# Performance work log

Measured on AMD Instinct MI355X. Metric: run time of the kernel, lower is better.

Reference implementation:

```python
import jax, jax.numpy as jnp
import numpy as np

# WikiText-103 adaptive softmax config
CUTOFFS = (0, 20000, 40000, 200000, 267735)  # cluster boundaries


def setup_inputs() -> dict:
    key = jax.random.key(0)
    ks = jax.random.split(key, 12)
    N, D = 1024, 1024
    rn = lambda k, shape, std: jax.random.normal(k, shape, jnp.float32) * std
    return {
        "hidden": jax.random.normal(ks[0], (N, D), jnp.float32),
        "target": jax.random.randint(ks[1], (N,), 0, CUTOFFS[-1], jnp.int32),
        "head_w": rn(ks[2], (20000, 1024), 0.02),
        "head_b": jnp.zeros((20000,), jnp.float32),
        "cluster_w": rn(ks[3], (3, 1024), 0.02),
        "cluster_b": jnp.zeros((3,), jnp.float32),
        "proj0": rn(ks[4], (1024, 1024), 0.01),
        "proj1": rn(ks[5], (1024, 256), 0.01),
        "proj2": rn(ks[6], (1024, 64), 0.01),
        "proj3": rn(ks[7], (1024, 16), 0.01),
        "w1": rn(ks[8], (20000, 256), 0.02),
        "b1": jnp.zeros((20000,), jnp.float32),
        "w2": rn(ks[9], (160000, 64), 0.02),
        "b2": jnp.zeros((160000,), jnp.float32),
        "w3": rn(ks[10], (67735, 16), 0.02),
        "b3": jnp.zeros((67735,), jnp.float32),
    }


def _logit(h, w, b, proj):
    # F.linear(F.linear(h, proj.t()), w, b) == (h @ proj) @ w.T + b
    return (h @ proj) @ w.T + b


def reference(hidden, target, head_w, head_b, cluster_w, cluster_b,
              proj0, proj1, proj2, proj3, w1, b1, w2, b2, w3, b3):
    # head: shortlist vocab (20000) + 3 cluster logits -> [N, 20003]
    hw = jnp.concatenate([head_w, cluster_w], axis=0)
    hb = jnp.concatenate([head_b, cluster_b], axis=0)
    head_lp = jax.nn.log_softmax(_logit(hidden, hw, hb, proj0), axis=-1)

    # cluster 0 (shortlist): logprob directly from head
    t0 = jnp.clip(target, 0, CUTOFFS[1] - 1)
    lp = jnp.take_along_axis(head_lp, t0[:, None].astype(jnp.int32), axis=1)[:, 0]

    tails = [(w1, b1, proj1), (w2, b2, proj2), (w3, b3, proj3)]
    for i, (w, b, p) in enumerate(tails, start=1):
        l, r = CUTOFFS[i], CUTOFFS[i + 1]
        mask = (target >= l) & (target < r)
        ti = jnp.clip(target - l, 0, r - l - 1)
        tail_lp = jax.nn.log_softmax(_logit(hidden, w, b, p), axis=-1)  # [N, r-l]
        # note: torch code indexes head_logprob[:, -i] (reversed cluster order quirk)
        lpi = head_lp[:, -i] + jnp.take_along_axis(tail_lp, ti[:, None], axis=1)[:, 0]
        lp = jnp.where(mask, lpi, lp)

    return -lp  # nll per token, keep_order semantics
```

## Files before the change

kernel.cpp:

```cpp
#include <hip/hip_runtime.h>
#include <math.h>

typedef __bf16 bf16;
typedef __bf16 bf16x4 __attribute__((ext_vector_type(4)));
typedef __bf16 bf16x8 __attribute__((ext_vector_type(8)));
typedef float  f32x4  __attribute__((ext_vector_type(4)));

__device__ __forceinline__ f32x4 mfma16x16x32(bf16x8 a, bf16x8 b, f32x4 c) {
  return __builtin_amdgcn_mfma_f32_16x16x32_bf16(a, b, c, 0, 0, 0);
}

__device__ __forceinline__ void async16(const bf16* gp, bf16* lp) {
  __builtin_amdgcn_global_load_lds(
      (const __attribute__((address_space(1))) void*)gp,
      (__attribute__((address_space(3))) void*)lp, 16, 0, 0);
}

__global__ void __launch_bounds__(256) convert_bf16_kernel(const float* __restrict__ in,
                                                           bf16* __restrict__ out, int n4) {
  int i = blockIdx.x * 256 + threadIdx.x;
  if (i < n4) {
    float4 f = ((const float4*)in)[i];
    bf16x4 b = {(bf16)f.x, (bf16)f.y, (bf16)f.z, (bf16)f.w};
    ((bf16x4*)out)[i] = b;
  }
}

__global__ void __launch_bounds__(256) convert_pad_kernel(const float* __restrict__ in,
                                                          bf16* __restrict__ out,
                                                          int n4, int n4tot) {
  int i = blockIdx.x * 256 + threadIdx.x;
  if (i >= n4tot) return;
  bf16x4 b = {(bf16)0.f, (bf16)0.f, (bf16)0.f, (bf16)0.f};
  if (i < n4) {
    float4 f = ((const float4*)in)[i];
    b = (bf16x4){(bf16)f.x, (bf16)f.y, (bf16)f.z, (bf16)f.w};
  }
  ((bf16x4*)out)[i] = b;
}

__global__ void __launch_bounds__(256) convert_w3_kernel(const float* __restrict__ w3,
                                                         bf16* __restrict__ W3b,
                                                         int n4, int n4tot) {
  int i = blockIdx.x * 256 + threadIdx.x;
  if (i >= n4tot) return;
  int row = i >> 2, kq = i & 3;
  bf16x4 z = {(bf16)0.f, (bf16)0.f, (bf16)0.f, (bf16)0.f};
  bf16x4 b = z;
  if (i < n4) {
    float4 f = *(const float4*)&w3[(size_t)i * 4];
    b = (bf16x4){(bf16)f.x, (bf16)f.y, (bf16)f.z, (bf16)f.w};
  }
  *(bf16x4*)&W3b[(size_t)row * 32 + kq * 4] = b;
  *(bf16x4*)&W3b[(size_t)row * 32 + 16 + kq * 4] = z;
}

__global__ void __launch_bounds__(256) transpose_convert_kernel(const float* __restrict__ P,
                                                                bf16* __restrict__ Pt, int dX) {
  __shared__ float t[32][33];
  int tx = threadIdx.x & 31, ty = threadIdx.x >> 5;
  int k0 = blockIdx.x * 32, c0 = blockIdx.y * 32;
#pragma unroll
  for (int s = 0; s < 4; ++s) {
    int k = k0 + ty + s * 8, col = c0 + tx;
    t[ty + s * 8][tx] = (col < dX) ? P[(size_t)k * dX + col] : 0.f;
  }
  __syncthreads();
#pragma unroll
  for (int s = 0; s < 4; ++s) {
    int colo = c0 + ty + s * 8;
    Pt[(size_t)colo * 1024 + k0 + tx] = (bf16)t[tx][ty + s * 8];
  }
}

__global__ void __launch_bounds__(1024) compact_kernel(const int* __restrict__ target,
                                                       int* __restrict__ rowmap,
                                                       int* __restrict__ slotmap,
                                                       int* __restrict__ counts) {
  __shared__ int cnt[3];
  int tid = threadIdx.x;
  if (tid < 3) cnt[tid] = 0;
  for (int i = tid; i < 3 * 1152; i += 1024) rowmap[i] = 0;
  __syncthreads();
  int t = target[tid];
  int c = (t >= 200000) ? 2 : (t >= 40000) ? 1 : (t >= 20000) ? 0 : -1;
  int slot = -1;
  if (c >= 0) {
    slot = atomicAdd(&cnt[c], 1);
    rowmap[c * 1152 + slot] = tid;
  }
  slotmap[tid] = slot;
  __syncthreads();
  if (tid < 3) counts[tid] = cnt[tid];
}

template <int KDIM, bool LSE>
__global__ void __launch_bounds__(256) gemm_kernel(
    const bf16* __restrict__ A, int strideA,
    const int* __restrict__ rmap, const int* __restrict__ cntp,
    const bf16* __restrict__ B,
    const float* __restrict__ bias, const float* __restrict__ bias2,
    int splice, int V, float* __restrict__ part, int nchunk,
    bf16* __restrict__ Out, int strideOut, int dX) {
  constexpr int BK = 64;
  constexpr int KG = BK / 8;
  constexpr int NIT = KDIM / BK;
  __shared__ bf16 Alds[2][128 * BK];
  __shared__ bf16 Blds[2][128 * BK];
  __shared__ float wpart[2][128];

  const int tid = threadIdx.x;
  const int w = tid >> 6, lane = tid & 63;
  const int q = lane >> 4, c = lane & 15;
  const int wr = w >> 1, wc = w & 1;

  int f = blockIdx.x;
  int xr = f & 7, rb = (f >> 3) & 7, cq = f >> 6;
  int chunk = cq * 8 + xr;
  if (chunk >= nchunk) return;
  const int row0 = rb * 128, col0 = chunk * 128;
  if (cntp && row0 >= *cntp) return;

  int arow[KG / 2];
#pragma unroll
  for (int i = 0; i < KG / 2; ++i) {
    int g = i * 256 + tid;
    int r = row0 + g / KG;
    arow[i] = rmap ? rmap[r] : r;
  }

  auto stage = [&](int kt, int pb) {
    const int k0 = kt * BK;
#pragma unroll
    for (int i = 0; i < KG / 2; ++i) {
      int g = i * 256 + tid;
      int col = g / KG, j = g % KG;
      int kg = j ^ (col & 7);
      async16(A + (size_t)arow[i] * strideA + k0 + kg * 8,
              &Alds[pb][(size_t)(g & ~63) * 8]);
      async16(B + (size_t)(col0 + col) * KDIM + k0 + kg * 8,
              &Blds[pb][(size_t)(g & ~63) * 8]);
    }
  };

  f32x4 acc[4][4] = {};

  stage(0, 0);
  __syncthreads();

  for (int kt = 0; kt < NIT; ++kt) {
    const int cb = kt & 1;
    if (kt + 1 < NIT) stage(kt + 1, cb ^ 1);
#pragma unroll
    for (int ks = 0; ks < BK / 32; ++ks) {
      bf16x8 af[4], bfr[4];
#pragma unroll
      for (int rt = 0; rt < 4; ++rt) {
        int rl = wr * 64 + rt * 16 + c;
        int kq = ks * 4 + q;
        int kg = kq ^ (rl & 7);
        af[rt] = *(const bf16x8*)&Alds[cb][((size_t)rl * KG + kg) * 8];
      }
#pragma unroll
      for (int ct = 0; ct < 4; ++ct) {
        int cl = wc * 64 + ct * 16 + c;
        int kq = ks * 4 + q;
        int kg = kq ^ (cl & 7);
        bfr[ct] = *(const bf16x8*)&Blds[cb][((size_t)cl * KG + kg) * 8];
      }
#pragma unroll
      for (int rt = 0; rt < 4; ++rt)
#pragma unroll
        for (int ct = 0; ct < 4; ++ct)
          acc[rt][ct] = mfma16x16x32(af[rt], bfr[ct], acc[rt][ct]);
    }
    __syncthreads();
  }

  if (!LSE) {
#pragma unroll
    for (int rt = 0; rt < 4; ++rt)
#pragma unroll
      for (int ct = 0; ct < 4; ++ct)
#pragma unroll
        for (int r = 0; r < 4; ++r) {
          int col = col0 + wc * 64 + ct * 16 + c;
          if (col < dX) {
            int row = row0 + wr * 64 + rt * 16 + q * 4 + r;
            Out[(size_t)row * strideOut + col] = (bf16)acc[rt][ct][r];
          }
        }
    return;
  }

  float bv[4];
#pragma unroll
  for (int ct = 0; ct < 4; ++ct) {
    int colg = col0 + wc * 64 + ct * 16 + c;
    bv[ct] = (colg < V) ? ((colg < splice) ? bias[colg] : bias2[colg - splice]) : -INFINITY;
  }
#pragma unroll
  for (int rt = 0; rt < 4; ++rt) {
#pragma unroll
    for (int r = 0; r < 4; ++r) {
      float s = 0.f;
#pragma unroll
      for (int ct = 0; ct < 4; ++ct) s += __expf(acc[rt][ct][r] + bv[ct]);
#pragma unroll
      for (int off = 1; off <= 8; off <<= 1) s += __shfl_xor(s, off);
      if (c == 0) wpart[wc][wr * 64 + rt * 16 + q * 4 + r] = s;
    }
  }
  __syncthreads();
  if (tid < 128)
    part[(size_t)chunk * 1024 + row0 + tid] = __logf(wpart[0][tid] + wpart[1][tid]);
}

template <int KDIM, int G>
__global__ void __launch_bounds__(256) gemm_lse_wide_kernel(
    const bf16* __restrict__ A, int strideA,
    const int* __restrict__ rmap, const int* __restrict__ cntp,
    const bf16* __restrict__ B, const float* __restrict__ bias,
    int V, float* __restrict__ part, int nchunk) {
  constexpr int BK = KDIM;
  constexpr int KG = BK / 8;
  constexpr int NL = KG / 2;
  __shared__ bf16 Alds[128 * BK];
  __shared__ bf16 Blds[3][128 * BK];
  __shared__ float biasl[G * 128];
  __shared__ float spart[2][128];

  const int tid = threadIdx.x;
  const int w = tid >> 6, lane = tid & 63;
  const int q = lane >> 4, c = lane & 15;
  const int wr = w >> 1, wc = w & 1;

  const int row0 = blockIdx.y * 128;
  if (row0 >= *cntp) return;
  const int chunk0 = blockIdx.x * G;
  const int nc = (nchunk - chunk0 < G) ? (nchunk - chunk0) : G;

  for (int i = tid; i < G * 128; i += 256) {
    int colg = chunk0 * 128 + i;
    biasl[i] = (colg < V) ? bias[colg] : -INFINITY;
  }
#pragma unroll
  for (int i = 0; i < NL; ++i) {
    int g = i * 256 + tid;
    int row = g / KG, j = g % KG;
    int kg = (KG == 8) ? (j ^ (row & 7)) : (j ^ ((row >> 1) & 3));
    int ar = rmap[row0 + row];
    async16(A + (size_t)ar * strideA + kg * 8, &Alds[(size_t)(g & ~63) * 8]);
  }
#pragma unroll
  for (int b = 0; b < 2; ++b) {
    int ck = (b < nc) ? b : nc - 1;
#pragma unroll
    for (int i = 0; i < NL; ++i) {
      int g = i * 256 + tid;
      int col = g / KG, j = g % KG;
      int kg = (KG == 8) ? (j ^ (col & 7)) : (j ^ ((col >> 1) & 3));
      async16(B + (size_t)((chunk0 + ck) * 128 + col) * KDIM + kg * 8,
              &Blds[b][(size_t)(g & ~63) * 8]);
    }
  }
  __syncthreads();

  bf16x8 af[BK / 32][4];
#pragma unroll
  for (int ks = 0; ks < BK / 32; ++ks)
#pragma unroll
    for (int rt = 0; rt < 4; ++rt) {
      int rl = wr * 64 + rt * 16 + c;
      int kq = ks * 4 + q;
      int kg = (KG == 8) ? (kq ^ (rl & 7)) : (kq ^ ((rl >> 1) & 3));
      af[ks][rt] = *(const bf16x8*)&Alds[((size_t)rl * KG + kg) * 8];
    }

  float sums[4][4] = {};
  int ib = 0;

  for (int ci = 0; ci < nc; ++ci) {
    {
      int pre = (ci + 2 < nc) ? ci + 2 : nc - 1;
      bf16* bw = Blds[(ib == 0) ? 2 : ib - 1];
#pragma unroll
      for (int i = 0; i < NL; ++i) {
        int g = i * 256 + tid;
        int col = g / KG, j = g % KG;
        int kg = (KG == 8) ? (j ^ (col & 7)) : (j ^ ((col >> 1) & 3));
        async16(B + (size_t)((chunk0 + pre) * 128 + col) * KDIM + kg * 8,
                &bw[(size_t)(g & ~63) * 8]);
      }
    }

    const bf16* Bl = Blds[ib];
    f32x4 acc[4][4] = {};
#pragma unroll
    for (int ks = 0; ks < BK / 32; ++ks) {
      bf16x8 bfr[4];
#pragma unroll
      for (int ct = 0; ct < 4; ++ct) {
        int cl = wc * 64 + ct * 16 + c;
        int kq = ks * 4 + q;
        int kg = (KG == 8) ? (kq ^ (cl & 7)) : (kq ^ ((cl >> 1) & 3));
        bfr[ct] = *(const bf16x8*)&Bl[((size_t)cl * KG + kg) * 8];
      }
#pragma unroll
      for (int rt = 0; rt < 4; ++rt)
#pragma unroll
        for (int ct = 0; ct < 4; ++ct)
          acc[rt][ct] = mfma16x16x32(af[ks][rt], bfr[ct], acc[rt][ct]);
    }

    float bv[4];
#pragma unroll
    for (int ct = 0; ct < 4; ++ct) bv[ct] = biasl[ci * 128 + wc * 64 + ct * 16 + c];
#pragma unroll
    for (int rt = 0; rt < 4; ++rt)
#pragma unroll
      for (int r = 0; r < 4; ++r) {
#pragma unroll
        for (int ct = 0; ct < 4; ++ct)
          sums[rt][r] += __expf(acc[rt][ct][r] + bv[ct]);
      }

    if constexpr (NL == 4) asm volatile("s_waitcnt vmcnt(4)" ::: "memory");
    else                   asm volatile("s_waitcnt vmcnt(2)" ::: "memory");
    __builtin_amdgcn_sched_barrier(0);
    __builtin_amdgcn_s_barrier();
    ib = (ib == 2) ? 0 : ib + 1;
  }

#pragma unroll
  for (int rt = 0; rt < 4; ++rt)
#pragma unroll
    for (int r = 0; r < 4; ++r) {
      float s = sums[rt][r];
#pragma unroll
      for (int off = 1; off <= 8; off <<= 1) s += __shfl_xor(s, off);
      if (c == 0) spart[wc][wr * 64 + rt * 16 + q * 4 + r] = s;
    }
  __syncthreads();
  if (tid < 128)
    part[(size_t)blockIdx.x * 1024 + row0 + tid] = __logf(spart[0][tid] + spart[1][tid]);
}

__device__ __forceinline__ float wave_sum64(float v) {
#pragma unroll
  for (int off = 1; off < 64; off <<= 1) v += __shfl_xor(v, off);
  return v;
}
__device__ float lse_cm(const float* __restrict__ p, int n, int idx) {
  int lane = threadIdx.x & 63;
  float s = 0.f;
  for (int i = lane; i < n; i += 64) s += __expf(p[(size_t)i * 1024 + idx]);
  s = wave_sum64(s);
  return __logf(s);
}
__device__ float dot_bw(const bf16* __restrict__ h, const float* __restrict__ wv, int K) {
  int lane = threadIdx.x & 63;
  float s = 0.f;
  for (int i = lane; i < K; i += 64) s += (float)h[i] * wv[i];
  return wave_sum64(s);
}

__global__ void __launch_bounds__(256) final_kernel(
    const int* __restrict__ target, const int* __restrict__ slotmap,
    const float* __restrict__ pH, const float* __restrict__ p1,
    const float* __restrict__ p2, const float* __restrict__ p3,
    const bf16* __restrict__ Hcat,
    const float* __restrict__ head_w, const float* __restrict__ head_b,
    const float* __restrict__ cluster_w, const float* __restrict__ cluster_b,
    const float* __restrict__ w1, const float* __restrict__ b1,
    const float* __restrict__ w2, const float* __restrict__ b2,
    const float* __restrict__ w3, const float* __restrict__ b3,
    float* __restrict__ out) {
  int wv = threadIdx.x >> 6, lane = threadIdx.x & 63;
  int row = blockIdx.x * 4 + wv;
  int t = target[row];
  const bf16* h0 = Hcat + (size_t)row * 1408;

  float lseH = lse_cm(pH, 157, row);
  float lp;
  if (t < 20000) {
    float sel = dot_bw(h0, head_w + (size_t)t * 1024, 1024) + head_b[t];
    lp = sel - lseH;
  } else {
    int i, L, KW, nch, hoff;
    const float* pp; const float* W; const float* Bb;
    if (t < 40000)        { i = 1; L = 20000;  KW = 256; nch = 157; hoff = 1024; pp = p1; W = w1; Bb = b1; }
    else if (t < 200000)  { i = 2; L = 40000;  KW = 64;  nch = 157; hoff = 1280; pp = p2; W = w2; Bb = b2; }
    else                  { i = 3; L = 200000; KW = 16;  nch = 67;  hoff = 1344; pp = p3; W = w3; Bb = b3; }
    int slot = slotmap[row];
    float lseT = lse_cm(pp, nch, slot);
    int ti = t - L;
    float tsel = dot_bw(h0 + hoff, W + (size_t)ti * KW, KW) + Bb[ti];
    int j = 3 - i;
    float csel = dot_bw(h0, cluster_w + (size_t)j * 1024, 1024) + cluster_b[j];
    lp = (csel - lseH) + (tsel - lseT);
  }
  if (lane == 0) out[row] = -lp;
}

extern "C" void kernel_launch(void* const* d_in, const int* in_sizes, int n_in,
                              void* d_out, int out_size, void* d_ws, size_t ws_size,
                              hipStream_t stream) {
  (void)in_sizes; (void)n_in; (void)out_size; (void)ws_size;
  const float* hidden    = (const float*)d_in[0];
  const int*   target    = (const int*)d_in[1];
  const float* head_w    = (const float*)d_in[2];
  const float* head_b    = (const float*)d_in[3];
  const float* cluster_w = (const float*)d_in[4];
  const float* cluster_b = (const float*)d_in[5];
  const float* proj0     = (const float*)d_in[6];
  const float* proj1     = (const float*)d_in[7];
  const float* proj2     = (const float*)d_in[8];
  const float* proj3     = (const float*)d_in[9];
  const float* w1 = (const float*)d_in[10];
  const float* b1 = (const float*)d_in[11];
  const float* w2 = (const float*)d_in[12];
  const float* b2 = (const float*)d_in[13];
  const float* w3 = (const float*)d_in[14];
  const float* b3 = (const float*)d_in[15];
  float* out = (float*)d_out;

  char* p = (char*)d_ws;
  bf16* hid_b = (bf16*)p; p += (size_t)1024 * 1024 * 2;
  bf16* Hcat  = (bf16*)p; p += (size_t)1024 * 1408 * 2;
  bf16* Pcat  = (bf16*)p; p += (size_t)1408 * 1024 * 2;
  bf16* Wh    = (bf16*)p; p += (size_t)20096 * 1024 * 2;
  bf16* W1b   = (bf16*)p; p += (size_t)20096 * 256 * 2;
  bf16* W2b   = (bf16*)p; p += (size_t)160000 * 64 * 2;
  bf16* W3b   = (bf16*)p; p += (size_t)67840 * 32 * 2;
  float* pH   = (float*)p; p += (size_t)157 * 1024 * 4;
  float* p1   = (float*)p; p += (size_t)157 * 1024 * 4;
  float* p2   = (float*)p; p += (size_t)1250 * 1024 * 4;
  float* p3   = (float*)p; p += (size_t)530 * 1024 * 4;
  int* rowmap = (int*)p;  p += 3 * 1152 * 4;
  int* slotmap= (int*)p;  p += 1024 * 4;
  int* counts = (int*)p;  p += 3 * 4;

  compact_kernel<<<1, 1024, 0, stream>>>(target, rowmap, slotmap, counts);

  convert_bf16_kernel<<<1024, 256, 0, stream>>>(hidden, hid_b, 262144);
  convert_bf16_kernel<<<20000, 256, 0, stream>>>(head_w, Wh, 5120000);
  convert_pad_kernel<<<96, 256, 0, stream>>>(cluster_w, Wh + (size_t)20000 * 1024, 768, 24576);
  convert_pad_kernel<<<5024, 256, 0, stream>>>(w1, W1b, 1280000, 1286144);
  convert_bf16_kernel<<<10000, 256, 0, stream>>>(w2, W2b, 2560000);
  convert_w3_kernel<<<1060, 256, 0, stream>>>(w3, W3b, 270940, 271360);
  transpose_convert_kernel<<<dim3(32, 32), 256, 0, stream>>>(proj0, Pcat, 1024);
  transpose_convert_kernel<<<dim3(32, 8), 256, 0, stream>>>(proj1, Pcat + (size_t)1024 * 1024, 256);
  transpose_convert_kernel<<<dim3(32, 2), 256, 0, stream>>>(proj2, Pcat + (size_t)1280 * 1024, 64);
  transpose_convert_kernel<<<dim3(32, 1), 256, 0, stream>>>(proj3, Pcat + (size_t)1344 * 1024, 16);

  gemm_kernel<1024, false><<<128, 256, 0, stream>>>(hid_b, 1024, nullptr, nullptr, Pcat,
                                                    nullptr, nullptr, 0, 0, nullptr, 11,
                                                    Hcat, 1408, 1376);

  gemm_kernel<1024, true><<<64 * 20, 256, 0, stream>>>(Hcat, 1408, nullptr, nullptr, Wh,
                                                       head_b, cluster_b, 20000, 20003,
                                                       pH, 157, nullptr, 0, 0);
  gemm_kernel<256, true><<<64 * 20, 256, 0, stream>>>(Hcat + 1024, 1408, rowmap, counts, W1b,
                                                      b1, b1, 0x40000000, 20000,
                                                      p1, 157, nullptr, 0, 0);

  gemm_lse_wide_kernel<64, 8><<<dim3(157, 8), 256, 0, stream>>>(
      Hcat + 1280, 1408, rowmap + 1152, counts + 1, W2b, b2, 160000, p2, 1250);
  gemm_lse_wide_kernel<32, 8><<<dim3(67, 8), 256, 0, stream>>>(
      Hcat + 1344, 1408, rowmap + 2304, counts + 2, W3b, b3, 67735, p3, 530);

  final_kernel<<<256, 256, 0, stream>>>(target, slotmap, pH, p1, p2, p3, Hcat,
                                        head_w, head_b, cluster_w, cluster_b,
                                        w1, b1, w2, b2, w3, b3, out);
}
```

Baseline: 407.0 us.

## Merge conversion launches and pipeline GEMM loads with partial vmcnt waits

The six fp32-to-bf16 conversion launches are merged into one kernel that picks its source by block index, and the four projection transposes become one launch, cutting launch overhead and the tail idle time between small kernels. The GEMM main loop now waits only until the current stage's async LDS loads land (vmcnt(8)) before a raw s_barrier, instead of a full __syncthreads drain, so the next tile's loads stay in flight during MFMA. It also raises wave priority around the MFMA block. The hand-written waitcnt depends on the exact number of outstanding loads per stage, and a wrong count could read stale LDS.

```diff
diff --git a/kernel.cpp b/kernel.cpp
--- a/kernel.cpp
+++ b/kernel.cpp
@@ -16,50 +16,50 @@
       (__attribute__((address_space(3))) void*)lp, 16, 0, 0);
 }
 
-__global__ void __launch_bounds__(256) convert_bf16_kernel(const float* __restrict__ in,
-                                                           bf16* __restrict__ out, int n4) {
-  int i = blockIdx.x * 256 + threadIdx.x;
+__global__ void __launch_bounds__(256) megaconvert_kernel(
+    const float* __restrict__ hidden, const float* __restrict__ head_w,
+    const float* __restrict__ cluster_w, const float* __restrict__ w1,
+    const float* __restrict__ w2, const float* __restrict__ w3,
+    bf16* __restrict__ hid_b, bf16* __restrict__ Wh, bf16* __restrict__ W1b,
+    bf16* __restrict__ W2b, bf16* __restrict__ W3b) {
+  int b = blockIdx.x;
+  const float* in; bf16* out; int n4, tot; int w3mode = 0;
+  if (b < 1024)       { in = hidden;    out = hid_b; n4 = 262144;  tot = 262144;  }
+  else if (b < 21024) { in = head_w;    out = Wh;    n4 = 5120000; tot = 5120000; b -= 1024; }
+  else if (b < 21120) { in = cluster_w; out = Wh + (size_t)20000 * 1024; n4 = 768; tot = 24576; b -= 21024; }
+  else if (b < 26144) { in = w1;        out = W1b;   n4 = 1280000; tot = 1286144; b -= 21120; }
+  else if (b < 36144) { in = w2;        out = W2b;   n4 = 2560000; tot = 2560000; b -= 26144; }
+  else                { in = w3;        out = W3b;   n4 = 270940;  tot = 271360;  b -= 36144; w3mode = 1; }
+  int i = b * 256 + threadIdx.x;
+  if (i >= tot) return;
+  bf16x4 z = {(bf16)0.f, (bf16)0.f, (bf16)0.f, (bf16)0.f};
+  bf16x4 v = z;
   if (i < n4) {
     float4 f = ((const float4*)in)[i];
-    bf16x4 b = {(bf16)f.x, (bf16)f.y, (bf16)f.z, (bf16)f.w};
-    ((bf16x4*)out)[i] = b;
-  }
-}
-
-__global__ void __launch_bounds__(256) convert_pad_kernel(const float* __restrict__ in,
-                                                          bf16* __restrict__ out,
-                                                          int n4, int n4tot) {
-  int i = blockIdx.x * 256 + threadIdx.x;
-  if (i >= n4tot) return;
-  bf16x4 b = {(bf16)0.f, (bf16)0.f, (bf16)0.f, (bf16)0.f};
-  if (i < n4) {
-    float4 f = ((const float4*)in)[i];
-    b = (bf16x4){(bf16)f.x, (bf16)f.y, (bf16)f.z, (bf16)f.w};
-  }
-  ((bf16x4*)out)[i] = b;
-}
-
-__global__ void __launch_bounds__(256) convert_w3_kernel(const float* __restrict__ w3,
-                                                         bf16* __restrict__ W3b,
-                                                         int n4, int n4tot) {
-  int i = blockIdx.x * 256 + threadIdx.x;
-  if (i >= n4tot) return;
-  int row = i >> 2, kq = i & 3;
-  bf16x4 z = {(bf16)0.f, (bf16)0.f, (bf16)0.f, (bf16)0.f};
-  bf16x4 b = z;
-  if (i < n4) {
-    float4 f = *(const float4*)&w3[(size_t)i * 4];
-    b = (bf16x4){(bf16)f.x, (bf16)f.y, (bf16)f.z, (bf16)f.w};
-  }
-  *(bf16x4*)&W3b[(size_t)row * 32 + kq * 4] = b;
-  *(bf16x4*)&W3b[(size_t)row * 32 + 16 + kq * 4] = z;
-}
-
-__global__ void __launch_bounds__(256) transpose_convert_kernel(const float* __restrict__ P,
-                                                                bf16* __restrict__ Pt, int dX) {
+    v = (bf16x4){(bf16)f.x, (bf16)f.y, (bf16)f.z, (bf16)f.w};
+  }
+  if (!w3mode) {
+    ((bf16x4*)out)[i] = v;
+  } else {
+    int row = i >> 2, kq = i & 3;
+    *(bf16x4*)&out[(size_t)row * 32 + kq * 4] = v;
+    *(bf16x4*)&out[(size_t)row * 32 + 16 + kq * 4] = z;
+  }
+}
+
+__global__ void __launch_bounds__(256) transpose_all_kernel(
+    const float* __restrict__ proj0, const float* __restrict__ proj1,
+    const float* __restrict__ proj2, const float* __restrict__ proj3,
+    bf16* __restrict__ Pcat) {
   __shared__ float t[32][33];
+  int y = blockIdx.y;
+  const float* P; bf16* Pt; int dX, cy;
+  if (y < 32)      { P = proj0; Pt = Pcat;                        dX = 1024; cy = y; }
+  else if (y < 40) { P = proj1; Pt = Pcat + (size_t)1024 * 1024;  dX = 256;  cy = y - 32; }
+  else if (y < 42) { P = proj2; Pt = Pcat + (size_t)1280 * 1024;  dX = 64;   cy = y - 40; }
+  else             { P = proj3; Pt = Pcat + (size_t)1344 * 1024;  dX = 16;   cy = y - 42; }
   int tx = threadIdx.x & 31, ty = threadIdx.x >> 5;
-  int k0 = blockIdx.x * 32, c0 = blockIdx.y * 32;
+  int k0 = blockIdx.x * 32, c0 = cy * 32;
 #pragma unroll
   for (int s = 0; s < 4; ++s) {
     int k = k0 + ty + s * 8, col = c0 + tx;
@@ -103,7 +103,7 @@
     int splice, int V, float* __restrict__ part, int nchunk,
     bf16* __restrict__ Out, int strideOut, int dX) {
   constexpr int BK = 64;
-  constexpr int KG = BK / 8;
+  constexpr int KG = 8;
   constexpr int NIT = KDIM / BK;
   __shared__ bf16 Alds[2][128 * BK];
   __shared__ bf16 Blds[2][128 * BK];
@@ -121,20 +121,20 @@
   const int row0 = rb * 128, col0 = chunk * 128;
   if (cntp && row0 >= *cntp) return;
 
-  int arow[KG / 2];
-#pragma unroll
-  for (int i = 0; i < KG / 2; ++i) {
+  int arow[4];
+#pragma unroll
+  for (int i = 0; i < 4; ++i) {
     int g = i * 256 + tid;
-    int r = row0 + g / KG;
+    int r = row0 + (g >> 3);
     arow[i] = rmap ? rmap[r] : r;
   }
 
   auto stage = [&](int kt, int pb) {
     const int k0 = kt * BK;
 #pragma unroll
-    for (int i = 0; i < KG / 2; ++i) {
+    for (int i = 0; i < 4; ++i) {
       int g = i * 256 + tid;
-      int col = g / KG, j = g % KG;
+      int col = g >> 3, j = g & 7;
       int kg = j ^ (col & 7);
       async16(A + (size_t)arow[i] * strideA + k0 + kg * 8,
               &Alds[pb][(size_t)(g & ~63) * 8]);
@@ -146,11 +146,18 @@
   f32x4 acc[4][4] = {};
 
   stage(0, 0);
-  __syncthreads();
-
   for (int kt = 0; kt < NIT; ++kt) {
     const int cb = kt & 1;
-    if (kt + 1 < NIT) stage(kt + 1, cb ^ 1);
+    if (kt + 1 < NIT) {
+      stage(kt + 1, cb ^ 1);
+      asm volatile("s_waitcnt vmcnt(8)" ::: "memory");
+    } else {
+      asm volatile("s_waitcnt vmcnt(0)" ::: "memory");
+    }
+    __builtin_amdgcn_sched_barrier(0);
+    __builtin_amdgcn_s_barrier();
+    asm volatile("" ::: "memory");
+    __builtin_amdgcn_s_setprio(1);
 #pragma unroll
     for (int ks = 0; ks < BK / 32; ++ks) {
       bf16x8 af[4], bfr[4];
@@ -174,7 +181,9 @@
         for (int ct = 0; ct < 4; ++ct)
           acc[rt][ct] = mfma16x16x32(af[rt], bfr[ct], acc[rt][ct]);
     }
-    __syncthreads();
+    __builtin_amdgcn_s_setprio(0);
+    asm volatile("" ::: "memory");
+    __builtin_amdgcn_s_barrier();
   }
 
   if (!LSE) {
@@ -443,16 +452,9 @@
 
   compact_kernel<<<1, 1024, 0, stream>>>(target, rowmap, slotmap, counts);
 
-  convert_bf16_kernel<<<1024, 256, 0, stream>>>(hidden, hid_b, 262144);
-  convert_bf16_kernel<<<20000, 256, 0, stream>>>(head_w, Wh, 5120000);
-  convert_pad_kernel<<<96, 256, 0, stream>>>(cluster_w, Wh + (size_t)20000 * 1024, 768, 24576);
-  convert_pad_kernel<<<5024, 256, 0, stream>>>(w1, W1b, 1280000, 1286144);
-  convert_bf16_kernel<<<10000, 256, 0, stream>>>(w2, W2b, 2560000);
-  convert_w3_kernel<<<1060, 256, 0, stream>>>(w3, W3b, 270940, 271360);
-  transpose_convert_kernel<<<dim3(32, 32), 256, 0, stream>>>(proj0, Pcat, 1024);
-  transpose_convert_kernel<<<dim3(32, 8), 256, 0, stream>>>(proj1, Pcat + (size_t)1024 * 1024, 256);
-  transpose_convert_kernel<<<dim3(32, 2), 256, 0, stream>>>(proj2, Pcat + (size_t)1280 * 1024, 64);
-  transpose_convert_kernel<<<dim3(32, 1), 256, 0, stream>>>(proj3, Pcat + (size_t)1344 * 1024, 16);
+  megaconvert_kernel<<<37204, 256, 0, stream>>>(hidden, head_w, cluster_w, w1, w2, w3,
+                                                hid_b, Wh, W1b, W2b, W3b);
+  transpose_all_kernel<<<dim3(32, 43), 256, 0, stream>>>(proj0, proj1, proj2, proj3, Pcat);
 
   gemm_kernel<1024, false><<<128, 256, 0, stream>>>(hid_b, 1024, nullptr, nullptr, Pcat,
                                                     nullptr, nullptr, 0, 0, nullptr, 11,
```

Result: faster. 382.8 us (-5.9%).
